# Kernel optimization log

Hardware: AMD Instinct MI355X
Metric: run time of the kernel (lower is better)

Reference implementation:

```python
import jax, jax.numpy as jnp
import numpy as np

HIDDEN = 128
N_LAYERS = 6
N_NODES = 50000
N_EDGES = 640000


def _glorot(key, shape):
    fan_in, fan_out = shape[0], shape[1]
    lim = (6.0 / (fan_in + fan_out)) ** 0.5
    return jax.random.uniform(key, shape, jnp.float32, -lim, lim)


def setup_inputs() -> dict:
    key = jax.random.key(0)
    ks = jax.random.split(key, 8)
    pos = jax.random.normal(ks[0], (N_NODES, 3), jnp.float32)
    edge_attr = jax.random.normal(ks[1], (N_EDGES, 3), jnp.float32)
    edge_index = jax.random.randint(ks[2], (2, N_EDGES), 0, N_NODES, jnp.int64)
    enc_w = _glorot(ks[3], (3, HIDDEN)); enc_b = jnp.zeros((HIDDEN,), jnp.float32)
    dec_w = _glorot(ks[4], (HIDDEN, 3)); dec_b = jnp.zeros((3,), jnp.float32)
    lk = jax.random.split(ks[5], 4 * N_LAYERS)
    edge_w1 = jnp.stack([_glorot(lk[4 * i + 0], (3 * HIDDEN, HIDDEN)) for i in range(N_LAYERS)])
    edge_w2 = jnp.stack([_glorot(lk[4 * i + 1], (HIDDEN, HIDDEN)) for i in range(N_LAYERS)])
    node_w1 = jnp.stack([_glorot(lk[4 * i + 2], (2 * HIDDEN, HIDDEN)) for i in range(N_LAYERS)])
    node_w2 = jnp.stack([_glorot(lk[4 * i + 3], (HIDDEN, HIDDEN)) for i in range(N_LAYERS)])
    edge_b1 = jnp.zeros((N_LAYERS, HIDDEN), jnp.float32)
    edge_b2 = jnp.zeros((N_LAYERS, HIDDEN), jnp.float32)
    node_b1 = jnp.zeros((N_LAYERS, HIDDEN), jnp.float32)
    node_b2 = jnp.zeros((N_LAYERS, HIDDEN), jnp.float32)
    return dict(pos=pos, edge_attr=edge_attr, edge_index=edge_index,
                enc_w=enc_w, enc_b=enc_b, dec_w=dec_w, dec_b=dec_b,
                edge_w1=edge_w1, edge_b1=edge_b1, edge_w2=edge_w2, edge_b2=edge_b2,
                node_w1=node_w1, node_b1=node_b1, node_w2=node_w2, node_b2=node_b2)


def _interaction(x, ef, src, dst, ew1, eb1, ew2, eb2, nw1, nb1, nw2, nb2, n_nodes):
    # message: concat(x_i=x[dst], x_j=x[src], edge_feature) -> edge MLP
    m = jnp.concatenate([x[dst], x[src], ef], axis=-1)            # [E, 3H]
    m = jax.nn.relu(m @ ew1 + eb1) @ ew2 + eb2                     # [E, H]
    # scatter-mean by target node
    sums = jax.ops.segment_sum(m, dst, num_segments=n_nodes)      # [N, H]
    cnt = jax.ops.segment_sum(jnp.ones((m.shape[0],), m.dtype), dst, num_segments=n_nodes)
    aggr = sums / jnp.maximum(cnt, 1.0)[:, None]
    node = jnp.concatenate([x, aggr], axis=-1)                     # [N, 2H]
    node = jax.nn.relu(node @ nw1 + nb1) @ nw2 + nb2               # [N, H]
    return x + node, ef + m


def reference(pos, edge_attr, edge_index, enc_w, enc_b, dec_w, dec_b,
              edge_w1, edge_b1, edge_w2, edge_b2,
              node_w1, node_b1, node_w2, node_b2):
    n_nodes = pos.shape[0]
    src = edge_index[0]
    dst = edge_index[1]
    x = jnp.zeros((n_nodes, HIDDEN), jnp.float32)
    ef = edge_attr @ enc_w + enc_b
    for i in range(N_LAYERS):
        x, ef = _interaction(x, ef, src, dst,
                             edge_w1[i], edge_b1[i], edge_w2[i], edge_b2[i],
                             node_w1[i], node_b1[i], node_w2[i], node_b2[i], n_nodes)
    out = x @ dec_w + dec_b                                        # [N, 3]
    # F.normalize(dim=1, eps=1e-12)
    norm = jnp.linalg.norm(out, axis=1, keepdims=True)
    return out / jnp.maximum(norm, 1e-12)
```

## Files before the change

kernel.cpp:

```cpp
#include <hip/hip_runtime.h>
#include <cstdint>

#define HIDDEN  128
#define NLAYERS 6
#define NNODES  50000
#define NEDGES  640000

typedef short short8 __attribute__((ext_vector_type(8)));
typedef float f32x4  __attribute__((ext_vector_type(4)));
typedef unsigned int   u32x4 __attribute__((ext_vector_type(4)));
typedef unsigned int   u32x2 __attribute__((ext_vector_type(2)));

__device__ __forceinline__ float bf2f(unsigned short u) {
    return __uint_as_float(((unsigned int)u) << 16);
}
__device__ __forceinline__ unsigned short f2bf(float f) {
    unsigned int u = __float_as_uint(f);
    unsigned int r = u + 0x7FFFu + ((u >> 16) & 1u);
    return (unsigned short)(r >> 16);
}
__device__ __forceinline__ unsigned int pack2(float a, float b) {
    unsigned int r;
    asm("v_cvt_pk_bf16_f32 %0, %1, %2" : "=v"(r) : "v"(a), "v"(b));
    return r;
}
__device__ __forceinline__ void unpack8u(u32x4 v, float* f) {
    f[0] = bf2f((unsigned short)(v.x & 0xffff)); f[1] = bf2f((unsigned short)(v.x >> 16));
    f[2] = bf2f((unsigned short)(v.y & 0xffff)); f[3] = bf2f((unsigned short)(v.y >> 16));
    f[4] = bf2f((unsigned short)(v.z & 0xffff)); f[5] = bf2f((unsigned short)(v.z >> 16));
    f[6] = bf2f((unsigned short)(v.w & 0xffff)); f[7] = bf2f((unsigned short)(v.w >> 16));
}

__device__ __forceinline__ void barrier_lgkm() {
    asm volatile("s_waitcnt lgkmcnt(0)" ::: "memory");
    __builtin_amdgcn_s_barrier();
    __builtin_amdgcn_sched_barrier(0);
}

__global__ void detect_kernel(const int* __restrict__ ei, int* __restrict__ flag)
{
    int lane = threadIdx.x;
    int v = ei[2 * lane + 1];
    unsigned long long b = __ballot(v != 0);
    if (lane == 0) *flag = (b != 0ULL) ? 1 : 0;
}

__global__ void normidx_kernel(const int* __restrict__ ei, const int* __restrict__ flag,
                               int* __restrict__ s32, int* __restrict__ d32)
{
    int e = blockIdx.x * blockDim.x + threadIdx.x;
    if (e >= NEDGES) return;
    int s, d;
    if (*flag) { s = ei[e]; d = ei[NEDGES + e]; }
    else       { s = ei[2 * e]; d = ei[2 * (NEDGES + e)]; }
    s32[e] = min(max(s, 0), NNODES - 1);
    d32[e] = min(max(d, 0), NNODES - 1);
}

__global__ void degree_kernel(const int* __restrict__ dst, int* __restrict__ deg)
{
    int e = blockIdx.x * blockDim.x + threadIdx.x;
    if (e < NEDGES) atomicAdd(&deg[dst[e]], 1);
}

#define SCAN_T 1024
__global__ void scan_kernel(const int* __restrict__ deg, int* __restrict__ off,
                            int* __restrict__ cursor)
{
    __shared__ int part[SCAN_T];
    const int t = threadIdx.x;
    const int CH = (NNODES + SCAN_T - 1) / SCAN_T;
    const int base = t * CH;
    int s = 0;
    for (int i = 0; i < CH; ++i) {
        int idx = base + i;
        if (idx < NNODES) s += deg[idx];
    }
    part[t] = s;
    __syncthreads();
    for (int d = 1; d < SCAN_T; d <<= 1) {
        int v = (t >= d) ? part[t - d] : 0;
        __syncthreads();
        part[t] += v;
        __syncthreads();
    }
    int run = (t == 0) ? 0 : part[t - 1];
    for (int i = 0; i < CH; ++i) {
        int idx = base + i;
        if (idx < NNODES) {
            off[idx] = run;
            cursor[idx] = run;
            run += deg[idx];
        }
    }
    if (t == SCAN_T - 1) off[NNODES] = run;
}

__global__ void scatter_kernel(const int* __restrict__ s32, const int* __restrict__ d32,
                               int* __restrict__ cursor,
                               int* __restrict__ sp, int* __restrict__ dp, int* __restrict__ ep)
{
    int e = blockIdx.x * blockDim.x + threadIdx.x;
    if (e >= NEDGES) return;
    int d = d32[e];
    int p = atomicAdd(&cursor[d], 1);
    sp[p] = s32[e];
    dp[p] = d;
    ep[p] = e;
}

__global__ void transpose_kernel(const float* __restrict__ W, unsigned short* __restrict__ WT,
                                 int K, int N, int L)
{
    long idx = (long)blockIdx.x * 256 + threadIdx.x;
    long tot = (long)L * K * N;
    if (idx >= tot) return;
    int kn = (int)(idx % ((long)K * N));
    int l  = (int)(idx / ((long)K * N));
    int k = kn / N;
    int n = kn % N;
    WT[(long)l * K * N + (long)n * K + k] = f2bf(W[idx]);
}

__global__ void encode_kernel(const float* __restrict__ ea,
                              const float* __restrict__ w,
                              const float* __restrict__ b,
                              const int* __restrict__ ep,
                              unsigned short* __restrict__ ef)
{
    int idx = blockIdx.x * blockDim.x + threadIdx.x;
    int p = idx >> 5;
    if (p >= NEDGES) return;
    int e = ep[p];
    int j = (idx & 31) << 2;
    float a0 = ea[e * 3 + 0], a1 = ea[e * 3 + 1], a2 = ea[e * 3 + 2];
    float4 w0 = *(const float4*)(w + 0 * HIDDEN + j);
    float4 w1 = *(const float4*)(w + 1 * HIDDEN + j);
    float4 w2 = *(const float4*)(w + 2 * HIDDEN + j);
    float4 bb = *(const float4*)(b + j);
    ushort4 o;
    o.x = f2bf(fmaf(a0, w0.x, fmaf(a1, w1.x, fmaf(a2, w2.x, bb.x))));
    o.y = f2bf(fmaf(a0, w0.y, fmaf(a1, w1.y, fmaf(a2, w2.y, bb.y))));
    o.z = f2bf(fmaf(a0, w0.z, fmaf(a1, w1.z, fmaf(a2, w2.z, bb.z))));
    o.w = f2bf(fmaf(a0, w0.w, fmaf(a1, w1.w, fmaf(a2, w2.w, bb.w))));
    *(ushort4*)(ef + (long)p * HIDDEN + j) = o;
}

__global__ __launch_bounds__(256, 3)
void edge_layer_mfma(const unsigned short* __restrict__ Xa,
                     const unsigned short* __restrict__ Xb,
                     unsigned short* __restrict__ ef,
                     float* __restrict__ sums,
                     const int* __restrict__ sp,
                     const int* __restrict__ dp,
                     const unsigned short* __restrict__ W1T,
                     const float* __restrict__ b1,
                     const unsigned short* __restrict__ W2T,
                     const float* __restrict__ b2,
                     const int flags)
{
    __shared__ __align__(16) unsigned char buf[45056];
    unsigned short* Hs = (unsigned short*)buf;
    unsigned short* Bs = (unsigned short*)(buf + 34816);
    __shared__ int dv[128];
    __shared__ int sv[128];

    const int tid = threadIdx.x;
    const int nwg = (int)gridDim.x;
    const int bid = (int)blockIdx.x;
    const int sb  = (bid & 7) * (nwg >> 3) + (bid >> 3);
    const long eb = (long)sb * 128;

    if (tid < 128) dv[tid]       = dp[eb + tid];
    else           sv[tid - 128] = sp[eb + tid - 128];

    const int lane = tid & 63;
    const int wv   = tid >> 6;
    const int mn   = lane & 15;
    const int q    = lane >> 4;
    const int bn   = tid >> 1;
    const int bk   = (tid & 1) << 4;

    u32x4 pw0, pw1;
    {
        const unsigned short* wp = W1T + (long)bn * 384 + 256 + bk;
        pw0 = *(const u32x4*)wp;
        pw1 = *(const u32x4*)(wp + 8);
    }

    short8 efold0[4], efold1[4];
    {
        const unsigned short* a0 = ef + (eb + wv * 32 + mn) * HIDDEN + (q << 3);
        const unsigned short* a1 = a0 + 16 * HIDDEN;
#pragma unroll
        for (int c = 0; c < 4; ++c) {
            efold0[c] = *(const short8*)(a0 + (c << 5));
            efold1[c] = *(const short8*)(a1 + (c << 5));
        }
    }

    f32x4 acc[2][8];
#pragma unroll
    for (int h = 0; h < 2; ++h)
#pragma unroll
        for (int t = 0; t < 8; ++t) acc[h][t] = (f32x4)0.0f;

    for (int c = 0; c < 4; ++c) {
        *(u32x4*)&Bs[bn * 40 + bk]     = pw0;
        *(u32x4*)&Bs[bn * 40 + bk + 8] = pw1;
        barrier_lgkm();
        if (c + 1 < 4) {
            const unsigned short* wp = W1T + (long)bn * 384 + 256 + ((c + 1) << 5) + bk;
            pw0 = *(const u32x4*)wp;
            pw1 = *(const u32x4*)(wp + 8);
        }
        short8 af0 = efold0[c];
        short8 af1 = efold1[c];
#pragma unroll
        for (int nt = 0; nt < 8; ++nt) {
            short8 bf = *(short8*)&Bs[(nt * 16 + mn) * 40 + (q << 3)];
            acc[0][nt] = __builtin_amdgcn_mfma_f32_16x16x32_bf16(af0, bf, acc[0][nt], 0, 0, 0);
            acc[1][nt] = __builtin_amdgcn_mfma_f32_16x16x32_bf16(af1, bf, acc[1][nt], 0, 0, 0);
        }
        barrier_lgkm();
    }

    if (flags & 1) {
#pragma unroll
        for (int h = 0; h < 2; ++h)
#pragma unroll
            for (int nt = 0; nt < 8; ++nt) {
                float b1v = b1[nt * 16 + mn];
#pragma unroll
                for (int r = 0; r < 4; r += 2) {
                    float h0 = fmaxf(acc[h][nt][r]     + b1v, 0.0f);
                    float h1 = fmaxf(acc[h][nt][r + 1] + b1v, 0.0f);
                    unsigned int p = pack2(h0, h1);
                    Hs[(wv * 32 + h * 16 + q * 4 + r)     * 136 + nt * 16 + mn] = (unsigned short)p;
                    Hs[(wv * 32 + h * 16 + q * 4 + r + 1) * 136 + nt * 16 + mn] = (unsigned short)(p >> 16);
                }
            }
    } else {
#pragma unroll
        for (int h = 0; h < 2; ++h)
#pragma unroll
            for (int nt = 0; nt < 8; ++nt)
#pragma unroll
                for (int r = 0; r < 4; r += 2) {
                    unsigned int p = pack2(acc[h][nt][r], acc[h][nt][r + 1]);
                    Hs[(wv * 32 + h * 16 + q * 4 + r)     * 136 + nt * 16 + mn] = (unsigned short)p;
                    Hs[(wv * 32 + h * 16 + q * 4 + r + 1) * 136 + nt * 16 + mn] = (unsigned short)(p >> 16);
                }

        {
            const int row  = wv * 32 + (lane >> 1);
            const int ch   = (lane & 1) << 6;
            const unsigned short* xap = Xa + (long)dv[row] * HIDDEN + ch;
            const unsigned short* xbp = Xb + (long)sv[row] * HIDDEN + ch;
            unsigned short* hp = &Hs[row * 136 + ch];
#pragma unroll
            for (int i = 0; i < 8; ++i) {
                u32x4 va = *(const u32x4*)(xap + (i << 3));
                u32x4 vb = *(const u32x4*)(xbp + (i << 3));
                u32x4 vp = *(u32x4*)(hp + (i << 3));
                float fa[8], fb[8], fp[8];
                unpack8u(va, fa); unpack8u(vb, fb); unpack8u(vp, fp);
                const float* bp = b1 + ch + (i << 3);
                u32x4 nw;
                float h0 = fmaxf(fp[0] + fa[0] + fb[0] + bp[0], 0.0f);
                float h1 = fmaxf(fp[1] + fa[1] + fb[1] + bp[1], 0.0f);
                float h2 = fmaxf(fp[2] + fa[2] + fb[2] + bp[2], 0.0f);
                float h3 = fmaxf(fp[3] + fa[3] + fb[3] + bp[3], 0.0f);
                float h4 = fmaxf(fp[4] + fa[4] + fb[4] + bp[4], 0.0f);
                float h5 = fmaxf(fp[5] + fa[5] + fb[5] + bp[5], 0.0f);
                float h6 = fmaxf(fp[6] + fa[6] + fb[6] + bp[6], 0.0f);
                float h7 = fmaxf(fp[7] + fa[7] + fb[7] + bp[7], 0.0f);
                nw.x = pack2(h0, h1); nw.y = pack2(h2, h3);
                nw.z = pack2(h4, h5); nw.w = pack2(h6, h7);
                *(u32x4*)(hp + (i << 3)) = nw;
            }
        }
    }

    f32x4 acc2[2][8];
#pragma unroll
    for (int h = 0; h < 2; ++h)
#pragma unroll
        for (int t = 0; t < 8; ++t) acc2[h][t] = (f32x4)0.0f;
    {
        const unsigned short* wp = W2T + (long)bn * 128 + bk;
        pw0 = *(const u32x4*)wp;
        pw1 = *(const u32x4*)(wp + 8);
    }
    for (int c = 0; c < 4; ++c) {
        *(u32x4*)&Bs[bn * 40 + bk]     = pw0;
        *(u32x4*)&Bs[bn * 40 + bk + 8] = pw1;
        barrier_lgkm();
        if (c + 1 < 4) {
            const unsigned short* wp = W2T + (long)bn * 128 + ((c + 1) << 5) + bk;
            pw0 = *(const u32x4*)wp;
            pw1 = *(const u32x4*)(wp + 8);
        }
        short8 af0 = *(short8*)&Hs[(wv * 32 + mn) * 136 + (c << 5) + (q << 3)];
        short8 af1 = *(short8*)&Hs[(wv * 32 + 16 + mn) * 136 + (c << 5) + (q << 3)];
#pragma unroll
        for (int nt = 0; nt < 8; ++nt) {
            short8 bf = *(short8*)&Bs[(nt * 16 + mn) * 40 + (q << 3)];
            acc2[0][nt] = __builtin_amdgcn_mfma_f32_16x16x32_bf16(af0, bf, acc2[0][nt], 0, 0, 0);
            acc2[1][nt] = __builtin_amdgcn_mfma_f32_16x16x32_bf16(af1, bf, acc2[1][nt], 0, 0, 0);
        }
        barrier_lgkm();
    }

#pragma unroll
    for (int h = 0; h < 2; ++h)
#pragma unroll
        for (int nt = 0; nt < 8; ++nt) {
            float b2v = b2[nt * 16 + mn];
#pragma unroll
            for (int r = 0; r < 4; r += 2) {
                unsigned int p = pack2(acc2[h][nt][r] + b2v, acc2[h][nt][r + 1] + b2v);
                Hs[(wv * 32 + h * 16 + q * 4 + r)     * 136 + nt * 16 + mn] = (unsigned short)p;
                Hs[(wv * 32 + h * 16 + q * 4 + r + 1) * 136 + nt * 16 + mn] = (unsigned short)(p >> 16);
            }
        }

    if (!(flags & 2)) {
#pragma unroll
        for (int h = 0; h < 2; ++h) {
            const int row = wv * 32 + h * 16 + mn;
            unsigned short* ep_ = ef + (eb + row) * HIDDEN + (q << 3);
#pragma unroll
            for (int c = 0; c < 4; ++c) {
                u32x4 mh = *(u32x4*)&Hs[row * 136 + (c << 5) + (q << 3)];
                float m[8], e[8];
                unpack8u(mh, m);
                short8 eo = h ? efold1[c] : efold0[c];
                u32x4 eu = *(u32x4*)&eo;
                unpack8u(eu, e);
                u32x4 nw;
                nw.x = pack2(e[0] + m[0], e[1] + m[1]);
                nw.y = pack2(e[2] + m[2], e[3] + m[3]);
                nw.z = pack2(e[4] + m[4], e[5] + m[5]);
                nw.w = pack2(e[6] + m[6], e[7] + m[7]);
                *(u32x4*)(ep_ + (c << 5)) = nw;
            }
        }
    }

    {
        const int cp = (tid & 63) << 1;
        const int qr = tid >> 6;
        float s0 = 0.0f, s1 = 0.0f;
        int cur = dv[qr * 32];
        for (int r = 0; r < 32; ++r) {
            const int row = qr * 32 + r;
            const int d = dv[row];
            if (d != cur) {
                atomicAdd(&sums[(long)cur * HIDDEN + cp], s0);
                atomicAdd(&sums[(long)cur * HIDDEN + cp + 1], s1);
                s0 = 0.0f; s1 = 0.0f;
                cur = d;
            }
            unsigned int u = *(unsigned int*)&Hs[row * 136 + cp];
            s0 += bf2f((unsigned short)(u & 0xffff));
            s1 += bf2f((unsigned short)(u >> 16));
        }
        atomicAdd(&sums[(long)cur * HIDDEN + cp], s0);
        atomicAdd(&sums[(long)cur * HIDDEN + cp + 1], s1);
    }
}

__global__ __launch_bounds__(512, 6)
void node_layer_mfma(float* __restrict__ x,
                     float* __restrict__ sums,
                     const int* __restrict__ deg,
                     const unsigned short* __restrict__ N1T,
                     const float* __restrict__ b1,
                     const unsigned short* __restrict__ N2T,
                     const float* __restrict__ b2,
                     const unsigned short* __restrict__ W1Tn,
                     unsigned short* __restrict__ Xa,
                     unsigned short* __restrict__ Xb,
                     const int first)
{
    __shared__ __align__(16) unsigned char nbuf[27648];
    unsigned short* As = (unsigned short*)nbuf;
    unsigned short* Hs = (unsigned short*)nbuf;
    unsigned short* Bs = (unsigned short*)(nbuf + 17408);
    __shared__ float cInv[64];

    const int tid = threadIdx.x;
    const long n0 = (long)blockIdx.x * 64;
    if (tid < 64) {
        long n = n0 + tid;
        cInv[tid] = (n < NNODES) ? 1.0f / fmaxf((float)deg[n], 1.0f) : 0.0f;
    }

    const int lane = tid & 63;
    const int wv   = tid >> 6;
    const int wb   = wv & 3;
    const int nh   = wv >> 2;
    const int mn   = lane & 15;
    const int q    = lane >> 4;
    const int srow = tid >> 3;
    const int ss   = tid & 7;
    const int bn   = tid >> 2;
    const int bk   = (tid & 3) << 3;

    long nr = n0 + srow;
    if (nr >= NNODES) nr = NNODES - 1;

    barrier_lgkm();

    f32x4 acc[4];
#pragma unroll
    for (int t = 0; t < 4; ++t) acc[t] = (f32x4)0.0f;

    const int c0 = first ? 4 : 0;

    float4 pa;
    u32x4 pb;
    {
        const float* base0 = first ? sums : x;
        const float* spx = base0 + nr * HIDDEN + (ss << 2);
        pa = *(const float4*)spx;
        const unsigned short* wp = N1T + (long)bn * 256 + (c0 << 5) + bk;
        pb = *(const u32x4*)wp;
    }
    float scCur = first ? cInv[srow] : 1.0f;
    for (int c = c0; c < 8; ++c) {
        {
            u32x2 w;
            w.x = pack2(pa.x * scCur, pa.y * scCur);
            w.y = pack2(pa.z * scCur, pa.w * scCur);
            *(u32x2*)&As[srow * 40 + (ss << 2)] = w;
        }
        *(u32x4*)&Bs[bn * 40 + bk] = pb;
        barrier_lgkm();
        if (c + 1 < 8) {
            const int cn = c + 1;
            const float* base = (cn < 4) ? x : sums;
            scCur = (cn < 4) ? 1.0f : cInv[srow];
            const float* spx = base + nr * HIDDEN + ((cn & 3) << 5) + (ss << 2);
            pa = *(const float4*)spx;
            const unsigned short* wp = N1T + (long)bn * 256 + (cn << 5) + bk;
            pb = *(const u32x4*)wp;
        }
        short8 af = *(short8*)&As[(wb * 16 + mn) * 40 + (q << 3)];
#pragma unroll
        for (int nt = 0; nt < 4; ++nt) {
            const int ntp = nh * 4 + nt;
            short8 bf = *(short8*)&Bs[(ntp * 16 + mn) * 40 + (q << 3)];
            acc[nt] = __builtin_amdgcn_mfma_f32_16x16x32_bf16(af, bf, acc[nt], 0, 0, 0);
        }
        barrier_lgkm();
    }

    if (W1Tn) {
        long row = n0 + srow;
        if (row < NNODES) {
            float4 z = make_float4(0.f, 0.f, 0.f, 0.f);
            float* p = sums + row * HIDDEN + (ss << 4);
#pragma unroll
            for (int i = 0; i < 4; ++i) ((float4*)p)[i] = z;
        }
    }

#pragma unroll
    for (int nt = 0; nt < 4; ++nt) {
        const int ntp = nh * 4 + nt;
        float b1v = b1[ntp * 16 + mn];
#pragma unroll
        for (int r = 0; r < 4; r += 2) {
            float h0 = fmaxf(acc[nt][r]     + b1v, 0.0f);
            float h1 = fmaxf(acc[nt][r + 1] + b1v, 0.0f);
            unsigned int p = pack2(h0, h1);
            Hs[(wb * 16 + q * 4 + r)     * 136 + ntp * 16 + mn] = (unsigned short)p;
            Hs[(wb * 16 + q * 4 + r + 1) * 136 + ntp * 16 + mn] = (unsigned short)(p >> 16);
        }
    }

    f32x4 acc2[4];
#pragma unroll
    for (int t = 0; t < 4; ++t) acc2[t] = (f32x4)0.0f;
    {
        const unsigned short* wp = N2T + (long)bn * 128 + bk;
        pb = *(const u32x4*)wp;
    }
    for (int c = 0; c < 4; ++c) {
        *(u32x4*)&Bs[bn * 40 + bk] = pb;
        barrier_lgkm();
        if (c + 1 < 4) {
            const unsigned short* wp = N2T + (long)bn * 128 + ((c + 1) << 5) + bk;
            pb = *(const u32x4*)wp;
        }
        short8 af = *(short8*)&Hs[(wb * 16 + mn) * 136 + (c << 5) + (q << 3)];
#pragma unroll
        for (int nt = 0; nt < 4; ++nt) {
            const int ntp = nh * 4 + nt;
            short8 bf = *(short8*)&Bs[(ntp * 16 + mn) * 40 + (q << 3)];
            acc2[nt] = __builtin_amdgcn_mfma_f32_16x16x32_bf16(af, bf, acc2[nt], 0, 0, 0);
        }
        barrier_lgkm();
    }

#pragma unroll
    for (int nt = 0; nt < 4; ++nt) {
        const int ntp = nh * 4 + nt;
        float b2v = b2[ntp * 16 + mn];
        float xns[4];
#pragma unroll
        for (int r = 0; r < 4; ++r) {
            long row = n0 + wb * 16 + q * 4 + r;
            float xn = 0.0f;
            if (row < NNODES) {
                float* p = x + row * HIDDEN + ntp * 16 + mn;
                xn = *p + acc2[nt][r] + b2v;
                *p = xn;
            }
            xns[r] = xn;
        }
        unsigned int p0 = pack2(xns[0], xns[1]);
        unsigned int p1 = pack2(xns[2], xns[3]);
        Hs[(wb * 16 + q * 4 + 0) * 136 + ntp * 16 + mn] = (unsigned short)p0;
        Hs[(wb * 16 + q * 4 + 1) * 136 + ntp * 16 + mn] = (unsigned short)(p0 >> 16);
        Hs[(wb * 16 + q * 4 + 2) * 136 + ntp * 16 + mn] = (unsigned short)p1;
        Hs[(wb * 16 + q * 4 + 3) * 136 + ntp * 16 + mn] = (unsigned short)(p1 >> 16);
    }

    if (W1Tn) {
#pragma unroll
        for (int half = 0; half < 2; ++half) {
            f32x4 accN[4];
#pragma unroll
            for (int t = 0; t < 4; ++t) accN[t] = (f32x4)0.0f;
            const int kbase = half << 7;
            {
                const unsigned short* wp = W1Tn + (long)bn * 384 + kbase + bk;
                pb = *(const u32x4*)wp;
            }
            for (int c = 0; c < 4; ++c) {
                *(u32x4*)&Bs[bn * 40 + bk] = pb;
                barrier_lgkm();
                if (c + 1 < 4) {
                    const unsigned short* wp = W1Tn + (long)bn * 384 + kbase + ((c + 1) << 5) + bk;
                    pb = *(const u32x4*)wp;
                }
                short8 af = *(short8*)&Hs[(wb * 16 + mn) * 136 + (c << 5) + (q << 3)];
#pragma unroll
                for (int nt = 0; nt < 4; ++nt) {
                    const int ntp = nh * 4 + nt;
                    short8 bf = *(short8*)&Bs[(ntp * 16 + mn) * 40 + (q << 3)];
                    accN[nt] = __builtin_amdgcn_mfma_f32_16x16x32_bf16(af, bf, accN[nt], 0, 0, 0);
                }
                barrier_lgkm();
            }
            unsigned short* Xout = half ? Xb : Xa;
#pragma unroll
            for (int nt = 0; nt < 4; ++nt) {
                const int ntp = nh * 4 + nt;
#pragma unroll
                for (int r = 0; r < 4; r += 2) {
                    unsigned int p = pack2(accN[nt][r], accN[nt][r + 1]);
                    long row0 = n0 + wb * 16 + q * 4 + r;
                    if (row0 < NNODES)
                        Xout[row0 * HIDDEN + ntp * 16 + mn] = (unsigned short)p;
                    if (row0 + 1 < NNODES)
                        Xout[(row0 + 1) * HIDDEN + ntp * 16 + mn] = (unsigned short)(p >> 16);
                }
            }
        }
    }
}

__global__ void decode_kernel(const float* __restrict__ x,
                              const float* __restrict__ w,
                              const float* __restrict__ b,
                              float* __restrict__ out)
{
    int gid = blockIdx.x * blockDim.x + threadIdx.x;
    int node = gid >> 6;
    int lane = threadIdx.x & 63;
    if (node >= NNODES) return;
    float a0 = 0.f, a1 = 0.f, a2 = 0.f;
#pragma unroll
    for (int k = lane; k < HIDDEN; k += 64) {
        float xv = x[(long)node * HIDDEN + k];
        a0 = fmaf(xv, w[k * 3 + 0], a0);
        a1 = fmaf(xv, w[k * 3 + 1], a1);
        a2 = fmaf(xv, w[k * 3 + 2], a2);
    }
#pragma unroll
    for (int off = 32; off > 0; off >>= 1) {
        a0 += __shfl_down(a0, off);
        a1 += __shfl_down(a1, off);
        a2 += __shfl_down(a2, off);
    }
    if (lane == 0) {
        a0 += b[0]; a1 += b[1]; a2 += b[2];
        float nrm = sqrtf(a0 * a0 + a1 * a1 + a2 * a2);
        float inv = 1.0f / fmaxf(nrm, 1e-12f);
        out[(long)node * 3 + 0] = a0 * inv;
        out[(long)node * 3 + 1] = a1 * inv;
        out[(long)node * 3 + 2] = a2 * inv;
    }
}

extern "C" void kernel_launch(void* const* d_in, const int* in_sizes, int n_in,
                              void* d_out, int out_size, void* d_ws, size_t ws_size,
                              hipStream_t stream)
{
    const float* edge_attr = (const float*)d_in[1];
    const int*   ei        = (const int*)d_in[2];
    const float* enc_w     = (const float*)d_in[3];
    const float* enc_b     = (const float*)d_in[4];
    const float* dec_w     = (const float*)d_in[5];
    const float* dec_b     = (const float*)d_in[6];
    const float* edge_w1   = (const float*)d_in[7];
    const float* edge_b1   = (const float*)d_in[8];
    const float* edge_w2   = (const float*)d_in[9];
    const float* edge_b2   = (const float*)d_in[10];
    const float* node_w1   = (const float*)d_in[11];
    const float* node_b1   = (const float*)d_in[12];
    const float* node_w2   = (const float*)d_in[13];
    const float* node_b2   = (const float*)d_in[14];

    char* ws = (char*)d_ws;
    unsigned short* ef  = (unsigned short*)(ws);
    float* x      = (float*)(ws + 163840000L);
    float* sums   = (float*)(ws + 189440000L);
    int*   src32  = (int*)  (ws + 215040000L);
    int*   dst32  = (int*)  (ws + 217600000L);
    int*   sp     = (int*)  (ws + 220160000L);
    int*   dp     = (int*)  (ws + 222720000L);
    int*   eperm  = (int*)  (ws + 225280000L);
    int*   deg    = (int*)  (ws + 227840000L);
    int*   off    = (int*)  (ws + 228040704L);
    int*   cursor = (int*)  (ws + 228241408L);
    int*   flag   = (int*)  (ws + 228442112L);
    unsigned short* W1T = (unsigned short*)(ws + 228442176L);
    unsigned short* W2T = (unsigned short*)(ws + 229032000L);
    unsigned short* N1T = (unsigned short*)(ws + 229228608L);
    unsigned short* N2T = (unsigned short*)(ws + 229621824L);
    unsigned short* Xa  = (unsigned short*)(ws + 229818432L);
    unsigned short* Xb  = (unsigned short*)(ws + 242618432L);

    float* out = (float*)d_out;

    hipMemsetAsync(x, 0, (size_t)NNODES * HIDDEN * sizeof(float), stream);
    hipMemsetAsync(sums, 0, (size_t)NNODES * HIDDEN * sizeof(float), stream);
    hipMemsetAsync(deg, 0, 200704, stream);

    detect_kernel<<<1, 64, 0, stream>>>(ei, flag);
    normidx_kernel<<<(NEDGES + 255) / 256, 256, 0, stream>>>(ei, flag, src32, dst32);
    degree_kernel<<<(NEDGES + 255) / 256, 256, 0, stream>>>(dst32, deg);
    scan_kernel<<<1, SCAN_T, 0, stream>>>(deg, off, cursor);
    scatter_kernel<<<(NEDGES + 255) / 256, 256, 0, stream>>>(src32, dst32, cursor, sp, dp, eperm);
    encode_kernel<<<(NEDGES * 32 + 255) / 256, 256, 0, stream>>>(edge_attr, enc_w, enc_b, eperm, ef);

    transpose_kernel<<<(6 * 384 * 128 + 255) / 256, 256, 0, stream>>>(edge_w1, W1T, 384, 128, 6);
    transpose_kernel<<<(6 * 128 * 128 + 255) / 256, 256, 0, stream>>>(edge_w2, W2T, 128, 128, 6);
    transpose_kernel<<<(6 * 256 * 128 + 255) / 256, 256, 0, stream>>>(node_w1, N1T, 256, 128, 6);
    transpose_kernel<<<(6 * 128 * 128 + 255) / 256, 256, 0, stream>>>(node_w2, N2T, 128, 128, 6);

    for (int l = 0; l < NLAYERS; ++l) {
        const int flags = (l == 0 ? 1 : 0) | (l == NLAYERS - 1 ? 2 : 0);
        edge_layer_mfma<<<NEDGES / 128, 256, 0, stream>>>(
            Xa, Xb, ef, sums, sp, dp,
            W1T + (long)l * 384 * 128, edge_b1 + (long)l * HIDDEN,
            W2T + (long)l * 128 * 128, edge_b2 + (long)l * HIDDEN, flags);
        const unsigned short* w1next = (l + 1 < NLAYERS) ? (W1T + (long)(l + 1) * 384 * 128) : nullptr;
        node_layer_mfma<<<(NNODES + 63) / 64, 512, 0, stream>>>(
            x, sums, deg,
            N1T + (long)l * 256 * 128, node_b1 + (long)l * HIDDEN,
            N2T + (long)l * 128 * 128, node_b2 + (long)l * HIDDEN,
            w1next, Xa, Xb, (l == 0) ? 1 : 0);
    }

    decode_kernel<<<(NNODES * 64 + 255) / 256, 256, 0, stream>>>(x, dec_w, dec_b, out);
}
```

Before: 1.441 ms.

## Split edge-layer work across 512 threads with one 16-row MFMA tile per wave

The edge-layer kernel moves from 256 to 512 threads per block. Each of the 8 waves now computes a single 16-edge MFMA tile instead of two, which roughly halves the accumulator and held-edge-feature registers per thread. Weight staging, the gather-add of node features and the scatter-sum atomics are re-partitioned across the larger thread count. The aim is higher occupancy and more latency hiding, at the cost of more barrier participants and more threads issuing the same LDS weight loads per block.

After: 1.445 ms. No clear change (+0.3%).

```diff
diff --git a/kernel.cpp b/kernel.cpp
--- a/kernel.cpp
+++ b/kernel.cpp
@@ -146,7 +146,7 @@
     *(ushort4*)(ef + (long)p * HIDDEN + j) = o;
 }
 
-__global__ __launch_bounds__(256, 3)
+__global__ __launch_bounds__(512, 6)
 void edge_layer_mfma(const unsigned short* __restrict__ Xa,
                      const unsigned short* __restrict__ Xb,
                      unsigned short* __restrict__ ef,
@@ -171,95 +171,80 @@
     const int sb  = (bid & 7) * (nwg >> 3) + (bid >> 3);
     const long eb = (long)sb * 128;
 
-    if (tid < 128) dv[tid]       = dp[eb + tid];
-    else           sv[tid - 128] = sp[eb + tid - 128];
+    if (tid < 128)      dv[tid]       = dp[eb + tid];
+    else if (tid < 256) sv[tid - 128] = sp[eb + tid - 128];
 
     const int lane = tid & 63;
     const int wv   = tid >> 6;
     const int mn   = lane & 15;
     const int q    = lane >> 4;
-    const int bn   = tid >> 1;
-    const int bk   = (tid & 1) << 4;
-
-    u32x4 pw0, pw1;
+    const int bn   = tid >> 2;
+    const int bk   = (tid & 3) << 3;
+
+    u32x4 pw0;
     {
         const unsigned short* wp = W1T + (long)bn * 384 + 256 + bk;
         pw0 = *(const u32x4*)wp;
-        pw1 = *(const u32x4*)(wp + 8);
-    }
-
-    short8 efold0[4], efold1[4];
+    }
+
+    short8 efold[4];
     {
-        const unsigned short* a0 = ef + (eb + wv * 32 + mn) * HIDDEN + (q << 3);
-        const unsigned short* a1 = a0 + 16 * HIDDEN;
-#pragma unroll
-        for (int c = 0; c < 4; ++c) {
-            efold0[c] = *(const short8*)(a0 + (c << 5));
-            efold1[c] = *(const short8*)(a1 + (c << 5));
-        }
-    }
-
-    f32x4 acc[2][8];
-#pragma unroll
-    for (int h = 0; h < 2; ++h)
-#pragma unroll
-        for (int t = 0; t < 8; ++t) acc[h][t] = (f32x4)0.0f;
+        const unsigned short* a0 = ef + (eb + wv * 16 + mn) * HIDDEN + (q << 3);
+#pragma unroll
+        for (int c = 0; c < 4; ++c) efold[c] = *(const short8*)(a0 + (c << 5));
+    }
+
+    f32x4 acc[8];
+#pragma unroll
+    for (int t = 0; t < 8; ++t) acc[t] = (f32x4)0.0f;
 
     for (int c = 0; c < 4; ++c) {
-        *(u32x4*)&Bs[bn * 40 + bk]     = pw0;
-        *(u32x4*)&Bs[bn * 40 + bk + 8] = pw1;
+        *(u32x4*)&Bs[bn * 40 + bk] = pw0;
         barrier_lgkm();
         if (c + 1 < 4) {
             const unsigned short* wp = W1T + (long)bn * 384 + 256 + ((c + 1) << 5) + bk;
             pw0 = *(const u32x4*)wp;
-            pw1 = *(const u32x4*)(wp + 8);
-        }
-        short8 af0 = efold0[c];
-        short8 af1 = efold1[c];
+        }
+        short8 af = efold[c];
 #pragma unroll
         for (int nt = 0; nt < 8; ++nt) {
             short8 bf = *(short8*)&Bs[(nt * 16 + mn) * 40 + (q << 3)];
-            acc[0][nt] = __builtin_amdgcn_mfma_f32_16x16x32_bf16(af0, bf, acc[0][nt], 0, 0, 0);
-            acc[1][nt] = __builtin_amdgcn_mfma_f32_16x16x32_bf16(af1, bf, acc[1][nt], 0, 0, 0);
+            acc[nt] = __builtin_amdgcn_mfma_f32_16x16x32_bf16(af, bf, acc[nt], 0, 0, 0);
         }
         barrier_lgkm();
     }
 
     if (flags & 1) {
 #pragma unroll
-        for (int h = 0; h < 2; ++h)
-#pragma unroll
-            for (int nt = 0; nt < 8; ++nt) {
-                float b1v = b1[nt * 16 + mn];
-#pragma unroll
-                for (int r = 0; r < 4; r += 2) {
-                    float h0 = fmaxf(acc[h][nt][r]     + b1v, 0.0f);
-                    float h1 = fmaxf(acc[h][nt][r + 1] + b1v, 0.0f);
-                    unsigned int p = pack2(h0, h1);
-                    Hs[(wv * 32 + h * 16 + q * 4 + r)     * 136 + nt * 16 + mn] = (unsigned short)p;
-                    Hs[(wv * 32 + h * 16 + q * 4 + r + 1) * 136 + nt * 16 + mn] = (unsigned short)(p >> 16);
-                }
-            }
+        for (int nt = 0; nt < 8; ++nt) {
+            float b1v = b1[nt * 16 + mn];
+#pragma unroll
+            for (int r = 0; r < 4; r += 2) {
+                float h0 = fmaxf(acc[nt][r]     + b1v, 0.0f);
+                float h1 = fmaxf(acc[nt][r + 1] + b1v, 0.0f);
+                unsigned int p = pack2(h0, h1);
+                Hs[(wv * 16 + q * 4 + r)     * 136 + nt * 16 + mn] = (unsigned short)p;
+                Hs[(wv * 16 + q * 4 + r + 1) * 136 + nt * 16 + mn] = (unsigned short)(p >> 16);
+            }
+        }
     } else {
 #pragma unroll
-        for (int h = 0; h < 2; ++h)
-#pragma unroll
-            for (int nt = 0; nt < 8; ++nt)
-#pragma unroll
-                for (int r = 0; r < 4; r += 2) {
-                    unsigned int p = pack2(acc[h][nt][r], acc[h][nt][r + 1]);
-                    Hs[(wv * 32 + h * 16 + q * 4 + r)     * 136 + nt * 16 + mn] = (unsigned short)p;
-                    Hs[(wv * 32 + h * 16 + q * 4 + r + 1) * 136 + nt * 16 + mn] = (unsigned short)(p >> 16);
-                }
+        for (int nt = 0; nt < 8; ++nt)
+#pragma unroll
+            for (int r = 0; r < 4; r += 2) {
+                unsigned int p = pack2(acc[nt][r], acc[nt][r + 1]);
+                Hs[(wv * 16 + q * 4 + r)     * 136 + nt * 16 + mn] = (unsigned short)p;
+                Hs[(wv * 16 + q * 4 + r + 1) * 136 + nt * 16 + mn] = (unsigned short)(p >> 16);
+            }
 
         {
-            const int row  = wv * 32 + (lane >> 1);
-            const int ch   = (lane & 1) << 6;
+            const int row = wv * 16 + (lane >> 2);
+            const int ch  = (lane & 3) << 5;
             const unsigned short* xap = Xa + (long)dv[row] * HIDDEN + ch;
             const unsigned short* xbp = Xb + (long)sv[row] * HIDDEN + ch;
             unsigned short* hp = &Hs[row * 136 + ch];
 #pragma unroll
-            for (int i = 0; i < 8; ++i) {
+            for (int i = 0; i < 4; ++i) {
                 u32x4 va = *(const u32x4*)(xap + (i << 3));
                 u32x4 vb = *(const u32x4*)(xbp + (i << 3));
                 u32x4 vp = *(u32x4*)(hp + (i << 3));
@@ -282,92 +267,76 @@
         }
     }
 
-    f32x4 acc2[2][8];
-#pragma unroll
-    for (int h = 0; h < 2; ++h)
-#pragma unroll
-        for (int t = 0; t < 8; ++t) acc2[h][t] = (f32x4)0.0f;
+    f32x4 acc2[8];
+#pragma unroll
+    for (int t = 0; t < 8; ++t) acc2[t] = (f32x4)0.0f;
     {
         const unsigned short* wp = W2T + (long)bn * 128 + bk;
         pw0 = *(const u32x4*)wp;
-        pw1 = *(const u32x4*)(wp + 8);
     }
     for (int c = 0; c < 4; ++c) {
-        *(u32x4*)&Bs[bn * 40 + bk]     = pw0;
-        *(u32x4*)&Bs[bn * 40 + bk + 8] = pw1;
+        *(u32x4*)&Bs[bn * 40 + bk] = pw0;
         barrier_lgkm();
         if (c + 1 < 4) {
             const unsigned short* wp = W2T + (long)bn * 128 + ((c + 1) << 5) + bk;
             pw0 = *(const u32x4*)wp;
-            pw1 = *(const u32x4*)(wp + 8);
-        }
-        short8 af0 = *(short8*)&Hs[(wv * 32 + mn) * 136 + (c << 5) + (q << 3)];
-        short8 af1 = *(short8*)&Hs[(wv * 32 + 16 + mn) * 136 + (c << 5) + (q << 3)];
+        }
+        short8 af = *(short8*)&Hs[(wv * 16 + mn) * 136 + (c << 5) + (q << 3)];
 #pragma unroll
         for (int nt = 0; nt < 8; ++nt) {
             short8 bf = *(short8*)&Bs[(nt * 16 + mn) * 40 + (q << 3)];
-            acc2[0][nt] = __builtin_amdgcn_mfma_f32_16x16x32_bf16(af0, bf, acc2[0][nt], 0, 0, 0);
-            acc2[1][nt] = __builtin_amdgcn_mfma_f32_16x16x32_bf16(af1, bf, acc2[1][nt], 0, 0, 0);
-        }
-        barrier_lgkm();
-    }
-
-#pragma unroll
-    for (int h = 0; h < 2; ++h)
-#pragma unroll
-        for (int nt = 0; nt < 8; ++nt) {
-            float b2v = b2[nt * 16 + mn];
-#pragma unroll
-            for (int r = 0; r < 4; r += 2) {
-                unsigned int p = pack2(acc2[h][nt][r] + b2v, acc2[h][nt][r + 1] + b2v);
-                Hs[(wv * 32 + h * 16 + q * 4 + r)     * 136 + nt * 16 + mn] = (unsigned short)p;
-                Hs[(wv * 32 + h * 16 + q * 4 + r + 1) * 136 + nt * 16 + mn] = (unsigned short)(p >> 16);
-            }
-        }
+            acc2[nt] = __builtin_amdgcn_mfma_f32_16x16x32_bf16(af, bf, acc2[nt], 0, 0, 0);
+        }
+        barrier_lgkm();
+    }
+
+#pragma unroll
+    for (int nt = 0; nt < 8; ++nt) {
+        float b2v = b2[nt * 16 + mn];
+#pragma unroll
+        for (int r = 0; r < 4; r += 2) {
+            unsigned int p = pack2(acc2[nt][r] + b2v, acc2[nt][r + 1] + b2v);
+            Hs[(wv * 16 + q * 4 + r)     * 136 + nt * 16 + mn] = (unsigned short)p;
+            Hs[(wv * 16 + q * 4 + r + 1) * 136 + nt * 16 + mn] = (unsigned short)(p >> 16);
+        }
+    }
 
     if (!(flags & 2)) {
-#pragma unroll
-        for (int h = 0; h < 2; ++h) {
-            const int row = wv * 32 + h * 16 + mn;
-            unsigned short* ep_ = ef + (eb + row) * HIDDEN + (q << 3);
-#pragma unroll
-            for (int c = 0; c < 4; ++c) {
-                u32x4 mh = *(u32x4*)&Hs[row * 136 + (c << 5) + (q << 3)];
-                float m[8], e[8];
-                unpack8u(mh, m);
-                short8 eo = h ? efold1[c] : efold0[c];
-                u32x4 eu = *(u32x4*)&eo;
-                unpack8u(eu, e);
-                u32x4 nw;
-                nw.x = pack2(e[0] + m[0], e[1] + m[1]);
-                nw.y = pack2(e[2] + m[2], e[3] + m[3]);
-                nw.z = pack2(e[4] + m[4], e[5] + m[5]);
-                nw.w = pack2(e[6] + m[6], e[7] + m[7]);
-                *(u32x4*)(ep_ + (c << 5)) = nw;
-            }
-        }
-    }
-
+        const int row = wv * 16 + mn;
+        unsigned short* ep_ = ef + (eb + row) * HIDDEN + (q << 3);
+#pragma unroll
+        for (int c = 0; c < 4; ++c) {
+            u32x4 mh = *(u32x4*)&Hs[row * 136 + (c << 5) + (q << 3)];
+            float m[8], e[8];
+            unpack8u(mh, m);
+            u32x4 eu = *(u32x4*)&efold[c];
+            unpack8u(eu, e);
+            u32x4 nw;
+            nw.x = pack2(e[0] + m[0], e[1] + m[1]);
+            nw.y = pack2(e[2] + m[2], e[3] + m[3]);
+            nw.z = pack2(e[4] + m[4], e[5] + m[5]);
+            nw.w = pack2(e[6] + m[6], e[7] + m[7]);
+            *(u32x4*)(ep_ + (c << 5)) = nw;
+        }
+    }
+
+    __syncthreads();
     {
-        const int cp = (tid & 63) << 1;
-        const int qr = tid >> 6;
-        float s0 = 0.0f, s1 = 0.0f;
+        const int qr = wv & 3;
+        const int ch = ((wv >> 2) << 6) + lane;
+        float s0 = 0.0f;
         int cur = dv[qr * 32];
         for (int r = 0; r < 32; ++r) {
             const int row = qr * 32 + r;
             const int d = dv[row];
             if (d != cur) {
-                atomicAdd(&sums[(long)cur * HIDDEN + cp], s0);
-                atomicAdd(&sums[(long)cur * HIDDEN + cp + 1], s1);
-                s0 = 0.0f; s1 = 0.0f;
+                atomicAdd(&sums[(long)cur * HIDDEN + ch], s0);
+                s0 = 0.0f;
                 cur = d;
             }
-            unsigned int u = *(unsigned int*)&Hs[row * 136 + cp];
-            s0 += bf2f((unsigned short)(u & 0xffff));
-            s1 += bf2f((unsigned short)(u >> 16));
-        }
-        atomicAdd(&sums[(long)cur * HIDDEN + cp], s0);
-        atomicAdd(&sums[(long)cur * HIDDEN + cp + 1], s1);
+            s0 += bf2f(Hs[row * 136 + ch]);
+        }
+        atomicAdd(&sums[(long)cur * HIDDEN + ch], s0);
     }
 }
 
@@ -666,7 +635,7 @@
 
     for (int l = 0; l < NLAYERS; ++l) {
         const int flags = (l == 0 ? 1 : 0) | (l == NLAYERS - 1 ? 2 : 0);
-        edge_layer_mfma<<<NEDGES / 128, 256, 0, stream>>>(
+        edge_layer_mfma<<<NEDGES / 128, 512, 0, stream>>>(
             Xa, Xb, ef, sums, sp, dp,
             W1T + (long)l * 384 * 128, edge_b1 + (long)l * HIDDEN,
             W2T + (long)l * 128 * 128, edge_b2 + (long)l * HIDDEN, flags);
```
